# Kernel tuning notes

Measured on AMD Instinct MI355X. Metric: run time of the kernel, lower is better.

## Reference

```python
import jax, jax.numpy as jnp
import numpy as np

EPS = 1e-12
HEADS = 16
DIM_KEYS = 16
DIM_VALUES = 64


def l2norm(t):
    # matches F.normalize(t, p=2, dim=-1) with eps=1e-12
    n = jnp.linalg.norm(t, axis=-1, keepdims=True)
    return t / jnp.maximum(n, EPS)


def tanh_norm(t):
    n = jnp.linalg.norm(t, axis=-1, keepdims=True)
    return jnp.tanh(n) * (t / jnp.maximum(n, EPS))


def split_heads(x, h):
    # [b, n, h*d] -> [b, h, n, d]
    b, n, hd = x.shape
    return x.reshape(b, n, h, hd // h).transpose(0, 2, 1, 3)


def setup_inputs() -> dict:
    key = jax.random.key(0)
    k1, k2, k3, k4 = jax.random.split(key, 4)
    b, n, dim = 4, 2048, 1024
    dim_inner = (DIM_KEYS + DIM_VALUES) * HEADS  # 1280
    tokens = jax.random.normal(k1, (b, n, dim), dtype=jnp.float32)
    Wqg = jax.random.normal(k2, (dim, dim_inner), dtype=jnp.float32) * (dim ** -0.5)
    Wkv = jax.random.normal(k3, (dim, dim_inner), dtype=jnp.float32) * (dim ** -0.5)
    Wout = jax.random.normal(k4, (DIM_VALUES * HEADS, dim), dtype=jnp.float32) * ((DIM_VALUES * HEADS) ** -0.5)
    return {"tokens": tokens, "Wqg": Wqg, "Wkv": Wkv, "Wout": Wout}


def reference(tokens, Wqg, Wkv, Wout):
    # self-attention variant: context = tokens, mask = None
    qg = split_heads(tokens @ Wqg, HEADS)   # [b, h, n, dk+dv]
    kv = split_heads(tokens @ Wkv, HEADS)
    queries, gates = qg[..., :DIM_KEYS], qg[..., DIM_KEYS:]
    keys, values = kv[..., :DIM_KEYS], kv[..., DIM_KEYS:]
    queries, keys, values = l2norm(queries), l2norm(keys), l2norm(values)
    sim = jnp.einsum('bhid,bhjd->bhij', queries, keys)
    attn = jnp.square(jax.nn.relu(sim))
    aggr = jnp.einsum('bhij,bhjd->bhid', attn, values)
    out = tanh_norm(aggr) * jnp.tanh(jax.nn.silu(gates))
    b, h, n, d = out.shape
    out = out.transpose(0, 2, 1, 3).reshape(b, n, h * d)  # merge heads
    return out @ Wout
```

## Files before the change

kernel.cpp:

```cpp
#include <hip/hip_runtime.h>
#include <cstdint>
#include <cstddef>

typedef __attribute__((ext_vector_type(8))) short short8;
typedef __attribute__((ext_vector_type(8))) unsigned short ushort8;
typedef __attribute__((ext_vector_type(4))) float f32x4;

#define DEV static __device__ __forceinline__

DEV unsigned short f2bf(float x) {
  union { float f; unsigned u; } v; v.f = x;
  unsigned r = v.u + 0x7fffu + ((v.u >> 16) & 1u);
  return (unsigned short)(r >> 16);
}
DEV float bf2f(unsigned short u) {
  union { unsigned u; float f; } v; v.u = ((unsigned)u) << 16;
  return v.f;
}
DEV unsigned pack2bf(float lo, float hi) {
  union { float f; unsigned u; } a, b; a.f = lo; b.f = hi;
  return __builtin_amdgcn_perm(b.u + 0x8000u, a.u + 0x8000u, 0x07060302u);
}
DEV f32x4 mfma16(short8 a, short8 b, f32x4 c) {
  return __builtin_amdgcn_mfma_f32_16x16x32_bf16(a, b, c, 0, 0, 0);
}

typedef __attribute__((address_space(1))) unsigned int g_u32;
typedef __attribute__((address_space(3))) unsigned int l_u32;
DEV void glds16(const unsigned short* g, unsigned short* l) {
  __builtin_amdgcn_global_load_lds((g_u32*)g, (l_u32*)l, 16, 0, 0);
}

constexpr int Bc = 4, Nc = 2048, Dc = 1024, Hc = 16, DKc = 16, DVc = 64, DIc = 1280;
constexpr int Mc = Bc * Nc;

__global__ __launch_bounds__(256) void convert_x(const float* __restrict__ X,
                                                 unsigned short* __restrict__ Xb, int total8) {
  int i = blockIdx.x * 256 + threadIdx.x;
  if (i >= total8) return;
  const float4* p = (const float4*)(X + (size_t)i * 8);
  float4 a = p[0], b = p[1];
  ushort8 o;
  o[0] = f2bf(a.x); o[1] = f2bf(a.y); o[2] = f2bf(a.z); o[3] = f2bf(a.w);
  o[4] = f2bf(b.x); o[5] = f2bf(b.y); o[6] = f2bf(b.z); o[7] = f2bf(b.w);
  *(ushort8*)(Xb + (size_t)i * 8) = o;
}

__global__ __launch_bounds__(256) void transpose_convert(const float* __restrict__ W,
                                                         unsigned short* __restrict__ WT,
                                                         int K, int N) {
  __shared__ unsigned short t[64][72];
  int k0 = blockIdx.x * 64, n0 = blockIdx.y * 64;
  int tid = threadIdx.x;
#pragma unroll
  for (int it = 0; it < 16; ++it) {
    int f = it * 256 + tid;
    int r = f >> 6, c = f & 63;
    t[c][r] = f2bf(W[(size_t)(k0 + r) * N + n0 + c]);
  }
  __syncthreads();
#pragma unroll
  for (int it = 0; it < 16; ++it) {
    int f = it * 256 + tid;
    int r = f >> 6, c = f & 63;
    WT[(size_t)(n0 + r) * K + k0 + c] = t[r][c];
  }
}

template <int OUT_BF16>
__global__ __launch_bounds__(256) void gemm_glds(const unsigned short* __restrict__ A,
                                                 const unsigned short* __restrict__ BT,
                                                 void* __restrict__ Cout,
                                                 int Mq, int Nq, int Kq) {
  __shared__ unsigned short As[128 * 64];
  __shared__ unsigned short Bs[128 * 64];
  int row0 = blockIdx.x * 128, col0 = blockIdx.y * 128;
  int tid = threadIdx.x, lane = tid & 63, wave = tid >> 6;
  int wm = wave >> 1, wn = wave & 1;
  int ql = lane >> 4, l16 = lane & 15;
  int r8 = lane >> 3, cbl = (lane & 7) ^ r8;

  const unsigned short* gA = A + (size_t)(row0 + wave * 32 + r8) * Kq + cbl * 8;
  const unsigned short* gB = BT + (size_t)(col0 + wave * 32 + r8) * Kq + cbl * 8;

  f32x4 acc[4][4];
#pragma unroll
  for (int i = 0; i < 4; i++)
#pragma unroll
    for (int j = 0; j < 4; j++) acc[i][j] = (f32x4){0.f, 0.f, 0.f, 0.f};

  for (int k0 = 0; k0 < Kq; k0 += 64) {
    __syncthreads();
#pragma unroll
    for (int i = 0; i < 4; ++i) {
      glds16(gA + (size_t)(i * 8) * Kq + k0, &As[(wave * 32 + i * 8) * 64]);
      glds16(gB + (size_t)(i * 8) * Kq + k0, &Bs[(wave * 32 + i * 8) * 64]);
    }
    __syncthreads();
#pragma unroll
    for (int kk = 0; kk < 64; kk += 32) {
      short8 af[4], bfr[4];
#pragma unroll
      for (int t = 0; t < 4; t++) {
        int row = wm * 64 + t * 16 + l16;
        int cb = (kk >> 3) + ql;
        af[t] = *(const short8*)&As[row * 64 + ((cb ^ (row & 7)) << 3)];
      }
#pragma unroll
      for (int t = 0; t < 4; t++) {
        int row = wn * 64 + t * 16 + l16;
        int cb = (kk >> 3) + ql;
        bfr[t] = *(const short8*)&Bs[row * 64 + ((cb ^ (row & 7)) << 3)];
      }
#pragma unroll
      for (int i = 0; i < 4; i++)
#pragma unroll
        for (int j = 0; j < 4; j++) acc[i][j] = mfma16(af[i], bfr[j], acc[i][j]);
    }
  }
#pragma unroll
  for (int i = 0; i < 4; i++)
#pragma unroll
    for (int j = 0; j < 4; j++)
#pragma unroll
      for (int r = 0; r < 4; r++) {
        int rr = row0 + wm * 64 + i * 16 + ql * 4 + r;
        int cc = col0 + wn * 64 + j * 16 + l16;
        if (OUT_BF16)
          ((unsigned short*)Cout)[(size_t)rr * Nq + cc] = f2bf(acc[i][j][r]);
        else
          ((float*)Cout)[(size_t)rr * Nq + cc] = acc[i][j][r];
      }
}

__global__ __launch_bounds__(256) void norm_kernel(const unsigned short* __restrict__ QG,
                                                   const unsigned short* __restrict__ KV,
                                                   unsigned short* __restrict__ Qn,
                                                   unsigned short* __restrict__ Kn,
                                                   unsigned short* __restrict__ Vtg) {
  int g = blockIdx.x * 256 + threadIdx.x;
  int n = g & (Nc - 1), bh = g >> 11;
  int h = bh & 15, b = bh >> 4;
  size_t src = ((size_t)(b * Nc + n)) * DIc + h * 80;

  {
    ushort8 u0 = *(const ushort8*)&QG[src];
    ushort8 u1 = *(const ushort8*)&QG[src + 8];
    float q[16], ss = 0.f;
#pragma unroll
    for (int i = 0; i < 8; i++) { q[i] = bf2f(u0[i]); q[8 + i] = bf2f(u1[i]); }
#pragma unroll
    for (int i = 0; i < 16; i++) ss += q[i] * q[i];
    float sc = 1.f / fmaxf(sqrtf(ss), 1e-12f);
    ushort8 o0, o1;
#pragma unroll
    for (int i = 0; i < 8; i++) { o0[i] = f2bf(q[i] * sc); o1[i] = f2bf(q[8 + i] * sc); }
    size_t dst = ((size_t)bh * Nc + n) * DKc;
    *(ushort8*)&Qn[dst] = o0;
    *(ushort8*)&Qn[dst + 8] = o1;
  }
  {
    ushort8 u0 = *(const ushort8*)&KV[src];
    ushort8 u1 = *(const ushort8*)&KV[src + 8];
    float q[16], ss = 0.f;
#pragma unroll
    for (int i = 0; i < 8; i++) { q[i] = bf2f(u0[i]); q[8 + i] = bf2f(u1[i]); }
#pragma unroll
    for (int i = 0; i < 16; i++) ss += q[i] * q[i];
    float sc = 1.f / fmaxf(sqrtf(ss), 1e-12f);
    ushort8 o0, o1;
#pragma unroll
    for (int i = 0; i < 8; i++) { o0[i] = f2bf(q[i] * sc); o1[i] = f2bf(q[8 + i] * sc); }
    size_t dst = ((size_t)bh * Nc + n) * DKc;
    *(ushort8*)&Kn[dst] = o0;
    *(ushort8*)&Kn[dst + 8] = o1;
  }
  {
    ushort8 u[8];
#pragma unroll
    for (int i = 0; i < 8; i++) u[i] = *(const ushort8*)&KV[src + 16 + i * 8];
    float ss = 0.f;
#pragma unroll
    for (int i = 0; i < 8; i++)
#pragma unroll
      for (int j = 0; j < 8; j++) { float x = bf2f(u[i][j]); ss += x * x; }
    float sc = 1.f / fmaxf(sqrtf(ss), 1e-12f);
#pragma unroll
    for (int i = 0; i < 8; i++)
#pragma unroll
      for (int j = 0; j < 8; j++) {
        int d = i * 8 + j;
        Vtg[((size_t)bh * DVc + d) * Nc + n] = f2bf(bf2f(u[i][j]) * sc);
      }
  }
}

__global__ __launch_bounds__(256, 4) void attn_kernel(const unsigned short* __restrict__ Qn,
                                                      const unsigned short* __restrict__ Kn,
                                                      const unsigned short* __restrict__ Vtg,
                                                      const unsigned short* __restrict__ QG,
                                                      unsigned short* __restrict__ outpre) {
  __shared__ unsigned short shm[2 * 64 * 128];

  int gid = blockIdx.x;
  int xcd = gid & 7, slot = gid >> 3;
  int bh = xcd * 8 + (slot & 7);
  int q0 = (slot >> 3) * 128;
  int b = bh >> 4, h = bh & 15;
  int tid = threadIdx.x, lane = tid & 63, wave = tid >> 6;
  int ql = lane >> 4, l16 = lane & 15;
  int qw0 = q0 + wave * 32;

  const short8 zz = {0, 0, 0, 0, 0, 0, 0, 0};

  short8 qf[2];
#pragma unroll
  for (int qt = 0; qt < 2; ++qt)
    qf[qt] = (ql < 2)
                 ? *(const short8*)&Qn[((size_t)bh * Nc + qw0 + qt * 16 + l16) * DKc + ql * 8]
                 : zz;

  const unsigned short* krow = Kn + ((size_t)bh * Nc) * DKc;
  const unsigned short* vbase = Vtg + ((size_t)bh * DVc) * Nc;

  int lr = lane >> 4, m16 = lane & 15;

  f32x4 acc[4][2];
#pragma unroll
  for (int dt = 0; dt < 4; dt++) { acc[dt][0] = (f32x4){0.f,0.f,0.f,0.f}; acc[dt][1] = (f32x4){0.f,0.f,0.f,0.f}; }

#pragma unroll
  for (int i = 0; i < 4; ++i) {
    int r0 = i * 16 + wave * 4;
    int d = r0 + lr;
    glds16(vbase + (size_t)d * Nc + 0 + ((m16 ^ (d & 7)) << 3), &shm[r0 * 128]);
  }

  for (int kt = 0; kt < Nc / 128; ++kt) {
    int k0 = kt * 128;
    unsigned short* vtb = &shm[(kt & 1) * 8192];
    __syncthreads();

    short8 kf[8];
#pragma unroll
    for (int kh = 0; kh < 8; ++kh)
      kf[kh] = (ql < 2)
                   ? *(const short8*)&krow[(size_t)(k0 + kh * 16 + l16) * DKc + ql * 8]
                   : zz;

    if (kt < Nc / 128 - 1) {
      unsigned short* nb = &shm[((kt + 1) & 1) * 8192];
      int kn0 = k0 + 128;
#pragma unroll
      for (int i = 0; i < 4; ++i) {
        int r0 = i * 16 + wave * 4;
        int d = r0 + lr;
        glds16(vbase + (size_t)d * Nc + kn0 + ((m16 ^ (d & 7)) << 3), &nb[r0 * 128]);
      }
    }

#pragma unroll
    for (int p = 0; p < 4; ++p) {
      f32x4 c0[2], c1[2];
#pragma unroll
      for (int qt = 0; qt < 2; ++qt) {
        c0[qt] = mfma16(kf[2 * p], qf[qt], (f32x4){0.f, 0.f, 0.f, 0.f});
        c1[qt] = mfma16(kf[2 * p + 1], qf[qt], (f32x4){0.f, 0.f, 0.f, 0.f});
      }
      short8 pf[2];
#pragma unroll
      for (int qt = 0; qt < 2; ++qt) {
        float a0 = fmaxf(c0[qt][0], 0.f); a0 *= a0;
        float a1 = fmaxf(c0[qt][1], 0.f); a1 *= a1;
        float a2 = fmaxf(c0[qt][2], 0.f); a2 *= a2;
        float a3 = fmaxf(c0[qt][3], 0.f); a3 *= a3;
        float b0 = fmaxf(c1[qt][0], 0.f); b0 *= b0;
        float b1 = fmaxf(c1[qt][1], 0.f); b1 *= b1;
        float b2 = fmaxf(c1[qt][2], 0.f); b2 *= b2;
        float b3 = fmaxf(c1[qt][3], 0.f); b3 *= b3;
        union { short8 s; uint4 u; } w;
        w.u.x = pack2bf(a0, a1);
        w.u.y = pack2bf(a2, a3);
        w.u.z = pack2bf(b0, b1);
        w.u.w = pack2bf(b2, b3);
        pf[qt] = w.s;
      }
      int tsw = (l16 & 7) << 1;
      int s1 = ((p * 8 + ql) ^ tsw) << 2;
      int s2 = ((p * 8 + 4 + ql) ^ tsw) << 2;
#pragma unroll
      for (int dt = 0; dt < 4; ++dt) {
        const unsigned short* vrow = vtb + (dt * 16 + l16) * 128;
        union { short8 s; uint4 u; } vf;
        uint2 va = *(const uint2*)&vrow[s1];
        uint2 vb2 = *(const uint2*)&vrow[s2];
        vf.u.x = va.x; vf.u.y = va.y; vf.u.z = vb2.x; vf.u.w = vb2.y;
#pragma unroll
        for (int qt = 0; qt < 2; ++qt) acc[dt][qt] = mfma16(vf.s, pf[qt], acc[dt][qt]);
      }
    }
  }

  __syncthreads();
  unsigned short(*of)[68] = (unsigned short(*)[68])shm;

#pragma unroll
  for (int qt = 0; qt < 2; ++qt) {
    float ss = 0.f;
#pragma unroll
    for (int dt = 0; dt < 4; ++dt)
#pragma unroll
      for (int r = 0; r < 4; ++r) { float v = acc[dt][qt][r]; ss += v * v; }
    ss += __shfl_xor(ss, 16, 64);
    ss += __shfl_xor(ss, 32, 64);
    float nrm = sqrtf(ss);
    float sc = tanhf(nrm) / fmaxf(nrm, 1e-12f);
    int q = qw0 + qt * 16 + l16;
    size_t gbase = ((size_t)(b * Nc + q)) * DIc + h * 80 + DKc;
#pragma unroll
    for (int dt = 0; dt < 4; ++dt) {
      uint2 gu = *(const uint2*)&QG[gbase + dt * 16 + ql * 4];
      float o[4];
#pragma unroll
      for (int r = 0; r < 4; ++r) {
        unsigned short gb = (r < 2) ? (unsigned short)(gu.x >> (16 * r))
                                    : (unsigned short)(gu.y >> (16 * (r - 2)));
        float x = bf2f(gb);
        float s = x / (1.f + __expf(-x));
        float e2 = __expf(2.f * s);
        float g = 1.f - 2.f / (e2 + 1.f);
        o[r] = acc[dt][qt][r] * sc * g;
      }
      uint2 w;
      w.x = pack2bf(o[0], o[1]);
      w.y = pack2bf(o[2], o[3]);
      *(uint2*)&of[wave * 32 + qt * 16 + l16][dt * 16 + ql * 4] = w;
    }
  }
  __syncthreads();
  {
    int row = tid >> 1, cb = (tid & 1) * 32;
    size_t obase = ((size_t)(b * Nc + q0 + row)) * (Hc * DVc) + h * DVc + cb;
#pragma unroll
    for (int i = 0; i < 4; ++i)
      *(ushort8*)&outpre[obase + i * 8] = *(const ushort8*)&of[row][cb + i * 8];
  }
}

extern "C" void kernel_launch(void* const* d_in, const int* in_sizes, int n_in,
                              void* d_out, int out_size, void* d_ws, size_t ws_size,
                              hipStream_t stream) {
  const float* X = (const float*)d_in[0];
  const float* Wqg = (const float*)d_in[1];
  const float* Wkv = (const float*)d_in[2];
  const float* Wout = (const float*)d_in[3];
  float* out = (float*)d_out;
  (void)in_sizes; (void)n_in; (void)out_size; (void)ws_size;

  char* ws = (char*)d_ws;
  size_t off = 0;
  auto alloc = [&](size_t bytes) {
    void* p = ws + off;
    off += (bytes + 255) & ~(size_t)255;
    return p;
  };
  unsigned short* Xbf   = (unsigned short*)alloc((size_t)Mc * Dc * 2);
  unsigned short* WqgT  = (unsigned short*)alloc((size_t)DIc * Dc * 2);
  unsigned short* WkvT  = (unsigned short*)alloc((size_t)DIc * Dc * 2);
  unsigned short* WoutT = (unsigned short*)alloc((size_t)Dc * Dc * 2);
  unsigned short* QG    = (unsigned short*)alloc((size_t)Mc * DIc * 2);
  unsigned short* KV    = (unsigned short*)alloc((size_t)Mc * DIc * 2);
  unsigned short* Qn    = (unsigned short*)alloc((size_t)Bc * Hc * Nc * DKc * 2);
  unsigned short* Kn    = (unsigned short*)alloc((size_t)Bc * Hc * Nc * DKc * 2);
  unsigned short* Vtg   = (unsigned short*)alloc((size_t)Bc * Hc * Nc * DVc * 2);
  unsigned short* outpre = Xbf;

  convert_x<<<(Mc * Dc / 8) / 256, 256, 0, stream>>>(X, Xbf, Mc * Dc / 8);
  transpose_convert<<<dim3(Dc / 64, DIc / 64), 256, 0, stream>>>(Wqg, WqgT, Dc, DIc);
  transpose_convert<<<dim3(Dc / 64, DIc / 64), 256, 0, stream>>>(Wkv, WkvT, Dc, DIc);
  transpose_convert<<<dim3(Dc / 64, Dc / 64), 256, 0, stream>>>(Wout, WoutT, Dc, Dc);
  gemm_glds<1><<<dim3(Mc / 128, DIc / 128), 256, 0, stream>>>(Xbf, WqgT, QG, Mc, DIc, Dc);
  gemm_glds<1><<<dim3(Mc / 128, DIc / 128), 256, 0, stream>>>(Xbf, WkvT, KV, Mc, DIc, Dc);
  norm_kernel<<<(Mc * Hc) / 256, 256, 0, stream>>>(QG, KV, Qn, Kn, Vtg);
  attn_kernel<<<1024, 256, 0, stream>>>(Qn, Kn, Vtg, QG, outpre);
  gemm_glds<0><<<dim3(Mc / 128, Dc / 128), 256, 0, stream>>>(outpre, WoutT, out, Mc, Dc, Dc);
}
```

Baseline: 268.5 us.

## Fuse QG/KV projections into one GEMM and run attention in fp16

The Q/G and K/V projection GEMMs become a single launch over a grid twice as wide. The kernel picks its destination buffer from the column offset and relies on WqgT and WkvT sitting contiguously in the workspace. Attention now uses fp16 MFMA, with the ReLU-square done in packed fp16 after a round-to-zero conversion, instead of scalar fp32 math plus manual bf16 packing. Q and K are stored zero-padded to 32 elements so fragment loads need no lane-conditional selects, at the cost of twice the Q/K storage and traffic and some fp16 rounding of the attention weights.

```diff
diff --git a/kernel.cpp b/kernel.cpp
--- a/kernel.cpp
+++ b/kernel.cpp
@@ -5,6 +5,8 @@
 typedef __attribute__((ext_vector_type(8))) short short8;
 typedef __attribute__((ext_vector_type(8))) unsigned short ushort8;
 typedef __attribute__((ext_vector_type(4))) float f32x4;
+typedef __attribute__((ext_vector_type(8))) _Float16 half8;
+typedef __attribute__((ext_vector_type(2))) __fp16 fp16x2;
 
 #define DEV static __device__ __forceinline__
 
@@ -23,6 +25,9 @@
 }
 DEV f32x4 mfma16(short8 a, short8 b, f32x4 c) {
   return __builtin_amdgcn_mfma_f32_16x16x32_bf16(a, b, c, 0, 0, 0);
+}
+DEV f32x4 mfma16h(half8 a, half8 b, f32x4 c) {
+  return __builtin_amdgcn_mfma_f32_16x16x32_f16(a, b, c, 0, 0, 0);
 }
 
 typedef __attribute__((address_space(1))) unsigned int g_u32;
@@ -67,10 +72,75 @@
   }
 }
 
-template <int OUT_BF16>
+__global__ __launch_bounds__(256) void gemm_proj(const unsigned short* __restrict__ A,
+                                                 const unsigned short* __restrict__ BT,
+                                                 unsigned short* __restrict__ QG,
+                                                 unsigned short* __restrict__ KV,
+                                                 int Kq) {
+  __shared__ unsigned short As[128 * 64];
+  __shared__ unsigned short Bs[128 * 64];
+  int row0 = blockIdx.x * 128, col0 = blockIdx.y * 128;
+  int tid = threadIdx.x, lane = tid & 63, wave = tid >> 6;
+  int wm = wave >> 1, wn = wave & 1;
+  int ql = lane >> 4, l16 = lane & 15;
+  int r8 = lane >> 3, cbl = (lane & 7) ^ r8;
+
+  unsigned short* dst = (col0 >= DIc) ? KV : QG;
+  int c0l = (col0 >= DIc) ? col0 - DIc : col0;
+
+  const unsigned short* gA = A + (size_t)(row0 + wave * 32 + r8) * Kq + cbl * 8;
+  const unsigned short* gB = BT + (size_t)(col0 + wave * 32 + r8) * Kq + cbl * 8;
+
+  f32x4 acc[4][4];
+#pragma unroll
+  for (int i = 0; i < 4; i++)
+#pragma unroll
+    for (int j = 0; j < 4; j++) acc[i][j] = (f32x4){0.f, 0.f, 0.f, 0.f};
+
+  for (int k0 = 0; k0 < Kq; k0 += 64) {
+    __syncthreads();
+#pragma unroll
+    for (int i = 0; i < 4; ++i) {
+      glds16(gA + (size_t)(i * 8) * Kq + k0, &As[(wave * 32 + i * 8) * 64]);
+      glds16(gB + (size_t)(i * 8) * Kq + k0, &Bs[(wave * 32 + i * 8) * 64]);
+    }
+    __syncthreads();
+#pragma unroll
+    for (int kk = 0; kk < 64; kk += 32) {
+      short8 af[4], bfr[4];
+#pragma unroll
+      for (int t = 0; t < 4; t++) {
+        int row = wm * 64 + t * 16 + l16;
+        int cb = (kk >> 3) + ql;
+        af[t] = *(const short8*)&As[row * 64 + ((cb ^ (row & 7)) << 3)];
+      }
+#pragma unroll
+      for (int t = 0; t < 4; t++) {
+        int row = wn * 64 + t * 16 + l16;
+        int cb = (kk >> 3) + ql;
+        bfr[t] = *(const short8*)&Bs[row * 64 + ((cb ^ (row & 7)) << 3)];
+      }
+#pragma unroll
+      for (int i = 0; i < 4; i++)
+#pragma unroll
+        for (int j = 0; j < 4; j++) acc[i][j] = mfma16(af[i], bfr[j], acc[i][j]);
+    }
+  }
+#pragma unroll
+  for (int i = 0; i < 4; i++)
+#pragma unroll
+    for (int j = 0; j < 4; j++)
+#pragma unroll
+      for (int r = 0; r < 4; r++) {
+        int rr = row0 + wm * 64 + i * 16 + ql * 4 + r;
+        int cc = c0l + wn * 64 + j * 16 + l16;
+        dst[(size_t)rr * DIc + cc] = f2bf(acc[i][j][r]);
+      }
+}
+
 __global__ __launch_bounds__(256) void gemm_glds(const unsigned short* __restrict__ A,
                                                  const unsigned short* __restrict__ BT,
-                                                 void* __restrict__ Cout,
+                                                 float* __restrict__ Cout,
                                                  int Mq, int Nq, int Kq) {
   __shared__ unsigned short As[128 * 64];
   __shared__ unsigned short Bs[128 * 64];
@@ -126,10 +196,7 @@
       for (int r = 0; r < 4; r++) {
         int rr = row0 + wm * 64 + i * 16 + ql * 4 + r;
         int cc = col0 + wn * 64 + j * 16 + l16;
-        if (OUT_BF16)
-          ((unsigned short*)Cout)[(size_t)rr * Nq + cc] = f2bf(acc[i][j][r]);
-        else
-          ((float*)Cout)[(size_t)rr * Nq + cc] = acc[i][j][r];
+        Cout[(size_t)rr * Nq + cc] = acc[i][j][r];
       }
 }
 
@@ -137,11 +204,13 @@
                                                    const unsigned short* __restrict__ KV,
                                                    unsigned short* __restrict__ Qn,
                                                    unsigned short* __restrict__ Kn,
-                                                   unsigned short* __restrict__ Vtg) {
+                                                   unsigned short* __restrict__ Vtg)
+{
   int g = blockIdx.x * 256 + threadIdx.x;
   int n = g & (Nc - 1), bh = g >> 11;
   int h = bh & 15, b = bh >> 4;
   size_t src = ((size_t)(b * Nc + n)) * DIc + h * 80;
+  const ushort8 zeros = {0, 0, 0, 0, 0, 0, 0, 0};
 
   {
     ushort8 u0 = *(const ushort8*)&QG[src];
@@ -152,12 +221,14 @@
 #pragma unroll
     for (int i = 0; i < 16; i++) ss += q[i] * q[i];
     float sc = 1.f / fmaxf(sqrtf(ss), 1e-12f);
-    ushort8 o0, o1;
-#pragma unroll
-    for (int i = 0; i < 8; i++) { o0[i] = f2bf(q[i] * sc); o1[i] = f2bf(q[8 + i] * sc); }
-    size_t dst = ((size_t)bh * Nc + n) * DKc;
-    *(ushort8*)&Qn[dst] = o0;
-    *(ushort8*)&Qn[dst + 8] = o1;
+    half8 o0, o1;
+#pragma unroll
+    for (int i = 0; i < 8; i++) { o0[i] = (_Float16)(q[i] * sc); o1[i] = (_Float16)(q[8 + i] * sc); }
+    size_t dst = ((size_t)bh * Nc + n) * 32;
+    *(half8*)&Qn[dst] = o0;
+    *(half8*)&Qn[dst + 8] = o1;
+    *(ushort8*)&Qn[dst + 16] = zeros;
+    *(ushort8*)&Qn[dst + 24] = zeros;
   }
   {
     ushort8 u0 = *(const ushort8*)&KV[src];
@@ -168,12 +239,14 @@
 #pragma unroll
     for (int i = 0; i < 16; i++) ss += q[i] * q[i];
     float sc = 1.f / fmaxf(sqrtf(ss), 1e-12f);
-    ushort8 o0, o1;
-#pragma unroll
-    for (int i = 0; i < 8; i++) { o0[i] = f2bf(q[i] * sc); o1[i] = f2bf(q[8 + i] * sc); }
-    size_t dst = ((size_t)bh * Nc + n) * DKc;
-    *(ushort8*)&Kn[dst] = o0;
-    *(ushort8*)&Kn[dst + 8] = o1;
+    half8 o0, o1;
+#pragma unroll
+    for (int i = 0; i < 8; i++) { o0[i] = (_Float16)(q[i] * sc); o1[i] = (_Float16)(q[8 + i] * sc); }
+    size_t dst = ((size_t)bh * Nc + n) * 32;
+    *(half8*)&Kn[dst] = o0;
+    *(half8*)&Kn[dst + 8] = o1;
+    *(ushort8*)&Kn[dst + 16] = zeros;
+    *(ushort8*)&Kn[dst + 24] = zeros;
   }
   {
     ushort8 u[8];
@@ -190,7 +263,9 @@
 #pragma unroll
       for (int j = 0; j < 8; j++) {
         int d = i * 8 + j;
-        Vtg[((size_t)bh * DVc + d) * Nc + n] = f2bf(bf2f(u[i][j]) * sc);
+        union { _Float16 h; unsigned short us; } cv;
+        cv.h = (_Float16)(bf2f(u[i][j]) * sc);
+        Vtg[((size_t)bh * DVc + d) * Nc + n] = cv.us;
       }
   }
 }
@@ -211,16 +286,12 @@
   int ql = lane >> 4, l16 = lane & 15;
   int qw0 = q0 + wave * 32;
 
-  const short8 zz = {0, 0, 0, 0, 0, 0, 0, 0};
-
-  short8 qf[2];
+  half8 qf[2];
 #pragma unroll
   for (int qt = 0; qt < 2; ++qt)
-    qf[qt] = (ql < 2)
-                 ? *(const short8*)&Qn[((size_t)bh * Nc + qw0 + qt * 16 + l16) * DKc + ql * 8]
-                 : zz;
-
-  const unsigned short* krow = Kn + ((size_t)bh * Nc) * DKc;
+    qf[qt] = *(const half8*)&Qn[((size_t)bh * Nc + qw0 + qt * 16 + l16) * 32 + ql * 8];
+
+  const unsigned short* krow = Kn + ((size_t)bh * Nc) * 32;
   const unsigned short* vbase = Vtg + ((size_t)bh * DVc) * Nc;
 
   int lr = lane >> 4, m16 = lane & 15;
@@ -241,12 +312,10 @@
     unsigned short* vtb = &shm[(kt & 1) * 8192];
     __syncthreads();
 
-    short8 kf[8];
+    half8 kf[8];
 #pragma unroll
     for (int kh = 0; kh < 8; ++kh)
-      kf[kh] = (ql < 2)
-                   ? *(const short8*)&krow[(size_t)(k0 + kh * 16 + l16) * DKc + ql * 8]
-                   : zz;
+      kf[kh] = *(const half8*)&krow[(size_t)(k0 + kh * 16 + l16) * 32 + ql * 8];
 
     if (kt < Nc / 128 - 1) {
       unsigned short* nb = &shm[((kt + 1) & 1) * 8192];
@@ -264,26 +333,23 @@
       f32x4 c0[2], c1[2];
 #pragma unroll
       for (int qt = 0; qt < 2; ++qt) {
-        c0[qt] = mfma16(kf[2 * p], qf[qt], (f32x4){0.f, 0.f, 0.f, 0.f});
-        c1[qt] = mfma16(kf[2 * p + 1], qf[qt], (f32x4){0.f, 0.f, 0.f, 0.f});
-      }
-      short8 pf[2];
+        c0[qt] = mfma16h(kf[2 * p], qf[qt], (f32x4){0.f, 0.f, 0.f, 0.f});
+        c1[qt] = mfma16h(kf[2 * p + 1], qf[qt], (f32x4){0.f, 0.f, 0.f, 0.f});
+      }
+      half8 pf[2];
 #pragma unroll
       for (int qt = 0; qt < 2; ++qt) {
-        float a0 = fmaxf(c0[qt][0], 0.f); a0 *= a0;
-        float a1 = fmaxf(c0[qt][1], 0.f); a1 *= a1;
-        float a2 = fmaxf(c0[qt][2], 0.f); a2 *= a2;
-        float a3 = fmaxf(c0[qt][3], 0.f); a3 *= a3;
-        float b0 = fmaxf(c1[qt][0], 0.f); b0 *= b0;
-        float b1 = fmaxf(c1[qt][1], 0.f); b1 *= b1;
-        float b2 = fmaxf(c1[qt][2], 0.f); b2 *= b2;
-        float b3 = fmaxf(c1[qt][3], 0.f); b3 *= b3;
-        union { short8 s; uint4 u; } w;
-        w.u.x = pack2bf(a0, a1);
-        w.u.y = pack2bf(a2, a3);
-        w.u.z = pack2bf(b0, b1);
-        w.u.w = pack2bf(b2, b3);
-        pf[qt] = w.s;
+        union { half8 h; fp16x2 p2[4]; } w;
+        fp16x2 t0 = __builtin_amdgcn_cvt_pkrtz(c0[qt][0], c0[qt][1]);
+        fp16x2 t1 = __builtin_amdgcn_cvt_pkrtz(c0[qt][2], c0[qt][3]);
+        fp16x2 t2 = __builtin_amdgcn_cvt_pkrtz(c1[qt][0], c1[qt][1]);
+        fp16x2 t3 = __builtin_amdgcn_cvt_pkrtz(c1[qt][2], c1[qt][3]);
+        const fp16x2 hz = {(__fp16)0, (__fp16)0};
+        t0 = __builtin_elementwise_max(t0, hz); w.p2[0] = t0 * t0;
+        t1 = __builtin_elementwise_max(t1, hz); w.p2[1] = t1 * t1;
+        t2 = __builtin_elementwise_max(t2, hz); w.p2[2] = t2 * t2;
+        t3 = __builtin_elementwise_max(t3, hz); w.p2[3] = t3 * t3;
+        pf[qt] = w.h;
       }
       int tsw = (l16 & 7) << 1;
       int s1 = ((p * 8 + ql) ^ tsw) << 2;
@@ -291,12 +357,12 @@
 #pragma unroll
       for (int dt = 0; dt < 4; ++dt) {
         const unsigned short* vrow = vtb + (dt * 16 + l16) * 128;
-        union { short8 s; uint4 u; } vf;
+        union { half8 s; uint4 u; } vf;
         uint2 va = *(const uint2*)&vrow[s1];
         uint2 vb2 = *(const uint2*)&vrow[s2];
         vf.u.x = va.x; vf.u.y = va.y; vf.u.z = vb2.x; vf.u.w = vb2.y;
 #pragma unroll
-        for (int qt = 0; qt < 2; ++qt) acc[dt][qt] = mfma16(vf.s, pf[qt], acc[dt][qt]);
+        for (int qt = 0; qt < 2; ++qt) acc[dt][qt] = mfma16h(vf.s, pf[qt], acc[dt][qt]);
       }
     }
   }
@@ -370,8 +436,8 @@
   unsigned short* WoutT = (unsigned short*)alloc((size_t)Dc * Dc * 2);
   unsigned short* QG    = (unsigned short*)alloc((size_t)Mc * DIc * 2);
   unsigned short* KV    = (unsigned short*)alloc((size_t)Mc * DIc * 2);
-  unsigned short* Qn    = (unsigned short*)alloc((size_t)Bc * Hc * Nc * DKc * 2);
-  unsigned short* Kn    = (unsigned short*)alloc((size_t)Bc * Hc * Nc * DKc * 2);
+  unsigned short* Qn    = (unsigned short*)alloc((size_t)Bc * Hc * Nc * 32 * 2);
+  unsigned short* Kn    = (unsigned short*)alloc((size_t)Bc * Hc * Nc * 32 * 2);
   unsigned short* Vtg   = (unsigned short*)alloc((size_t)Bc * Hc * Nc * DVc * 2);
   unsigned short* outpre = Xbf;
 
@@ -379,9 +445,8 @@
   transpose_convert<<<dim3(Dc / 64, DIc / 64), 256, 0, stream>>>(Wqg, WqgT, Dc, DIc);
   transpose_convert<<<dim3(Dc / 64, DIc / 64), 256, 0, stream>>>(Wkv, WkvT, Dc, DIc);
   transpose_convert<<<dim3(Dc / 64, Dc / 64), 256, 0, stream>>>(Wout, WoutT, Dc, Dc);
-  gemm_glds<1><<<dim3(Mc / 128, DIc / 128), 256, 0, stream>>>(Xbf, WqgT, QG, Mc, DIc, Dc);
-  gemm_glds<1><<<dim3(Mc / 128, DIc / 128), 256, 0, stream>>>(Xbf, WkvT, KV, Mc, DIc, Dc);
+  gemm_proj<<<dim3(Mc / 128, 2 * DIc / 128), 256, 0, stream>>>(Xbf, WqgT, QG, KV, Dc);
   norm_kernel<<<(Mc * Hc) / 256, 256, 0, stream>>>(QG, KV, Qn, Kn, Vtg);
   attn_kernel<<<1024, 256, 0, stream>>>(Qn, Kn, Vtg, QG, outpre);
-  gemm_glds<0><<<dim3(Mc / 128, Dc / 128), 256, 0, stream>>>(outpre, WoutT, out, Mc, Dc, Dc);
-}
+  gemm_glds<<<dim3(Mc / 128, Dc / 128), 256, 0, stream>>>(outpre, WoutT, out, Mc, Dc, Dc);
+}
```

Result: faster. 256.7 us (-4.4%).
